# Performance work log

Measured on AMD Instinct MI355X. Metric: run time of the kernel, lower is better.

The kernel has to match this reference:

```python
import math
import jax, jax.numpy as jnp
import numpy as np

B, L, E, H, NL = 8, 512, 512, 8, 2


def setup_inputs() -> dict:
    key = jax.random.key(0)
    ks = jax.random.split(key, 12)
    s = 0.02  # weight init scale
    return {
        "inputs_4e": jax.random.normal(ks[0], (B, L, 4 * E), jnp.float32),
        "query_embed": jax.random.normal(ks[1], (B, L, E), jnp.float32),
        "rel": jax.random.normal(ks[2], (B, L, L), jnp.float32),
        "resp_rel": jax.random.normal(ks[3], (B, L, L), jnp.float32),
        "timestamp": jax.random.uniform(ks[4], (B, L, L), jnp.float32) * 10.0,
        "l1": jax.random.uniform(ks[5], (1,), jnp.float32),
        "l2": jax.random.uniform(ks[6], (1,), jnp.float32),
        "l3": jax.random.uniform(ks[7], (1,), jnp.float32),
        "Win": jax.random.normal(ks[8], (4 * E, E), jnp.float32) * s,
        "b_in": jnp.zeros((E,), jnp.float32),
        "Wqkv": jax.random.normal(ks[9], (NL, 3, E, E), jnp.float32) * s,
        "bqkv": jnp.zeros((NL, 3, E), jnp.float32),
        "Wf1": jax.random.normal(ks[10], (2 * E, E), jnp.float32) * s,
        "bf1": jnp.zeros((E,), jnp.float32),
        "Wf2": jax.random.normal(ks[11], (E, 1), jnp.float32) * s,
        "bf2": jnp.zeros((1,), jnp.float32),
    }


def _mha(q_in, k_in, v_in, Wq, bq, Wk, bk, Wv, bv,
         rel, resp_rel, timestamp, l1, l2, l3, mask):
    Bb, Ll, Ee = q_in.shape
    d = Ee // H

    def split(x, W, b):  # (B,L,E) -> (B,H,L,d)
        return (x @ W + b).reshape(Bb, Ll, H, d).transpose(0, 2, 1, 3)

    q = split(q_in, Wq, bq)
    k = split(k_in, Wk, bk)
    v = split(v_in, Wv, bv)

    # relation softmax: zero out where mask==False, -1e4 at zeros
    maskf = mask.astype(rel.dtype)              # (1,1,L,L)
    rel_m = rel[:, None, :, :] * maskf          # (B,1,L,L), broadcasts over heads
    rel_attn = jax.nn.softmax(jnp.where(rel_m == 0, -1e4, rel_m), axis=-1)
    resp_m = resp_rel[:, None, :, :] * maskf
    resp_attn = jax.nn.softmax(jnp.where(resp_m == 0, -1e4, resp_m), axis=-1)

    # QK softmax with causal mask
    scores = jnp.einsum('bhqd,bhkd->bhqk', q, k) / math.sqrt(d)
    scores = jnp.where(mask, -1e9, scores)
    prob_attn = jax.nn.softmax(scores, axis=-1)

    # time-decay softmax
    ts = jnp.exp(-jnp.abs(timestamp))[:, None, :, :]  # (B,1,L,L)
    ts = jnp.where(mask, -jnp.inf, ts)
    time_attn = jax.nn.softmax(ts, axis=-1)

    # blend (ablation flags all True)
    p = (1.0 - l2) * prob_attn + l2 * time_attn
    p = (1.0 - l1) * p + l1 * rel_attn
    p = (1.0 - l3) * p + l3 * resp_attn

    out = jnp.einsum('bhqk,bhkd->bhqd', p, v)
    out = out.transpose(0, 2, 1, 3).reshape(Bb, Ll, Ee)
    return out, p


def reference(inputs_4e, query_embed, rel, resp_rel, timestamp,
              l1, l2, l3, Win, b_in, Wqkv, bqkv, Wf1, bf1, Wf2, bf2):
    mask = jnp.triu(jnp.ones((1, 1, L, L), dtype=bool), k=1)  # future mask
    inputs = jax.nn.relu(inputs_4e @ Win + b_in)              # lin_in_interaction

    outputs, attn = _mha(query_embed, inputs, inputs,
                         Wqkv[0, 0], bqkv[0, 0], Wqkv[0, 1], bqkv[0, 1],
                         Wqkv[0, 2], bqkv[0, 2],
                         rel, resp_rel, timestamp, l1, l2, l3, mask)
    for i in range(1, NL):
        residual, attn = _mha(query_embed, outputs, outputs,
                              Wqkv[i, 0], bqkv[i, 0], Wqkv[i, 1], bqkv[i, 1],
                              Wqkv[i, 2], bqkv[i, 2],
                              rel, resp_rel, timestamp, l1, l2, l3, mask)
        outputs = outputs + jax.nn.relu(residual)

    concat_q = jnp.concatenate([outputs, query_embed], axis=-1)  # (B,L,2E)
    h = jax.nn.relu(concat_q @ Wf1 + bf1)
    return h @ Wf2 + bf2  # (B,L,1)
```

## Files before the change

### kernel.cpp

```cpp
#include <hip/hip_runtime.h>
#include <math.h>

namespace {
constexpr int B = 8, L = 512, E = 512, H = 8;
constexpr int M = B * L;
}

typedef float f32x4 __attribute__((ext_vector_type(4)));
typedef short bf16x8 __attribute__((ext_vector_type(8)));

__device__ inline ushort f2b(float f) {
  unsigned u = __float_as_uint(f);
  u += 0x7FFF + ((u >> 16) & 1);
  return (ushort)(u >> 16);
}
__device__ inline float b2f(ushort h) { return __uint_as_float(((unsigned)h) << 16); }

__device__ inline f32x4 mfma16(bf16x8 a, bf16x8 b, f32x4 c) {
  return __builtin_amdgcn_mfma_f32_16x16x32_bf16(a, b, c, 0, 0, 0);
}

__device__ __forceinline__ void gl2lds16(const ushort* g, ushort* l) {
  __builtin_amdgcn_global_load_lds(
      (const __attribute__((address_space(1))) void*)g,
      (__attribute__((address_space(3))) void*)l, 16, 0, 0);
}

template <int NROWS>
__device__ __forceinline__ void stage64(const ushort* __restrict__ g, int ldg,
                                        ushort* lds, int tid) {
  const int w = tid >> 6, l = tid & 63;
  constexpr int RPW = NROWS / 4;
  constexpr int NI = RPW / 8;
#pragma unroll
  for (int it = 0; it < NI; ++it) {
    const int rbase = w * RPW + it * 8;
    const int row = rbase + (l >> 3);
    const int chunk = (l & 7) ^ (row & 7);
    gl2lds16(g + (size_t)row * ldg + chunk * 8, lds + rbase * 64);
  }
}

template <int BM, int NBUF>
__device__ __forceinline__ void stage_comb(const ushort* b0, const ushort* b1,
                                           const ushort* b2, const ushort* b3,
                                           ushort* lds, int tid) {
#pragma unroll
  for (int it = 0; it < BM / 32; ++it) {
    const int row = (tid >> 3) + it * 32;
    const int slot = tid & 7;
    const size_t off = (size_t)row * 512 + slot * 8;
    union Uu { uint4 u; ushort s[8]; } va, vb, vc, vd, vo;
    va.u = *(const uint4*)(b0 + off);
    vb.u = *(const uint4*)(b1 + off);
    if (NBUF == 4) {
      vc.u = *(const uint4*)(b2 + off);
      vd.u = *(const uint4*)(b3 + off);
    }
#pragma unroll
    for (int e = 0; e < 8; ++e) {
      float f = b2f(va.s[e]) + b2f(vb.s[e]);
      if (NBUF == 4) f += fmaxf(b2f(vc.s[e]) + b2f(vd.s[e]), 0.f);
      vo.s[e] = f2b(f);
    }
    *(uint4*)(&lds[row * 64 + ((slot ^ (row & 7)) * 8)]) = vo.u;
  }
}

template <int BM, int MODE, int HAS_BIAS, int ACT, int STAGEA>
__device__ __forceinline__ void dev_gemm(
    ushort* lds, int bxx, int by, const ushort* A, const ushort* A2,
    const ushort* A3, const ushort* A4, const ushort* Aq,
    const ushort* Wt, const float* bias, ushort* C0, ushort* C1, ushort* C2,
    ushort* C3, int K, int N) {
  ushort* Als = lds;
  ushort* Bls = lds + 2 * BM * 64;
  const int tid = threadIdx.x;
  const int l = tid & 63, wv = tid >> 6;
  const int wr = wv >> 1, wc = wv & 1;
  const int g = l >> 4, c = l & 15;
  constexpr int WM = BM / 2;
  constexpr int MFR = WM / 16;
  const int bm = by * BM;
  const int bn64 = bxx * 64;
  const int sec = (MODE == 3 || MODE == 5) ? (bn64 >> 9) : 0;
  const bool vsec = (MODE == 3 && sec == 2) || (MODE == 5 && sec == 1);

  const ushort* Ause = A;
  if (MODE == 3 && (sec == 1 || sec == 2)) Ause = A2;
  const int ldA = K;
  const ushort* Bp = Wt + (size_t)bn64 * K;

  f32x4 acc[MFR][2];
#pragma unroll
  for (int mi = 0; mi < MFR; ++mi)
#pragma unroll
    for (int ni = 0; ni < 2; ++ni) acc[mi][ni] = f32x4{0.f, 0.f, 0.f, 0.f};

  auto stageA = [&](int t, int buf) {
    ushort* dst = Als + buf * BM * 64;
    if (STAGEA == 0) {
      stage64<BM>(Ause + (size_t)bm * ldA + t * 64, ldA, dst, tid);
    } else if (STAGEA == 2) {
      stage_comb<BM, 2>(A + (size_t)bm * 512 + t * 64,
                        A2 + (size_t)bm * 512 + t * 64, nullptr, nullptr, dst, tid);
    } else {
      if (t < 8)
        stage_comb<BM, 4>(A + (size_t)bm * 512 + t * 64,
                          A2 + (size_t)bm * 512 + t * 64,
                          A3 + (size_t)bm * 512 + t * 64,
                          A4 + (size_t)bm * 512 + t * 64, dst, tid);
      else
        stage64<BM>(Aq + (size_t)bm * 512 + (t - 8) * 64, 512, dst, tid);
    }
  };

  stageA(0, 0);
  stage64<64>(Bp, K, Bls, tid);
  __syncthreads();

  const int NT = K >> 6;
  int cur = 0;
  for (int t = 0; t < NT; ++t) {
    if (t + 1 < NT) {
      stageA(t + 1, cur ^ 1);
      stage64<64>(Bp + (t + 1) * 64, K, Bls + (cur ^ 1) * 64 * 64, tid);
    }
#pragma unroll
    for (int ks = 0; ks < 2; ++ks) {
      bf16x8 af[MFR], bf_[2];
#pragma unroll
      for (int mi = 0; mi < MFR; ++mi) {
        const int row = wr * WM + mi * 16 + c;
        af[mi] = *(const bf16x8*)(&Als[cur * BM * 64 + row * 64 +
                                       (((ks * 4 + g) ^ (row & 7)) * 8)]);
      }
#pragma unroll
      for (int ni = 0; ni < 2; ++ni) {
        const int row = wc * 32 + ni * 16 + c;
        bf_[ni] = *(const bf16x8*)(&Bls[cur * 64 * 64 + row * 64 +
                                        (((ks * 4 + g) ^ (row & 7)) * 8)]);
      }
      if (vsec) {
#pragma unroll
        for (int mi = 0; mi < MFR; ++mi)
#pragma unroll
          for (int ni = 0; ni < 2; ++ni)
            acc[mi][ni] = mfma16(bf_[ni], af[mi], acc[mi][ni]);
      } else {
#pragma unroll
        for (int mi = 0; mi < MFR; ++mi)
#pragma unroll
          for (int ni = 0; ni < 2; ++ni)
            acc[mi][ni] = mfma16(af[mi], bf_[ni], acc[mi][ni]);
      }
    }
    __syncthreads();
    cur ^= 1;
  }

  if (vsec) {
    const int vbase = (MODE == 3) ? 1024 : 512;
    const int e0 = bn64 - vbase;
#pragma unroll
    for (int ni = 0; ni < 2; ++ni) {
#pragma unroll
      for (int r = 0; r < 4; ++r) {
        const int e = e0 + wc * 32 + ni * 16 + g * 4 + r;
        const float bv = HAS_BIAS ? bias[vbase + e] : 0.f;
#pragma unroll
        for (int mi = 0; mi < MFR; ++mi) {
          const int m = bm + wr * WM + mi * 16 + c;
          const int bb = m >> 9, lt = m & 511;
          C2[((size_t)bb * 512 + e) * 512 + lt] = f2b(acc[mi][ni][r] + bv);
        }
      }
    }
  } else {
    ushort* dst = C0;
    int nsub = 0, ldc = N;
    if (MODE == 3 || MODE == 5) {
      dst = (MODE == 5) ? C1 : (sec == 0 ? C0 : (sec == 1 ? C1 : C3));
      nsub = sec * 512;
      ldc = 512;
    }
#pragma unroll
    for (int ni = 0; ni < 2; ++ni) {
      const int n = bn64 + wc * 32 + ni * 16 + c;
      const float bv = HAS_BIAS ? bias[n] : 0.f;
#pragma unroll
      for (int mi = 0; mi < MFR; ++mi) {
#pragma unroll
        for (int r = 0; r < 4; ++r) {
          const int m = bm + wr * WM + mi * 16 + g * 4 + r;
          float v = acc[mi][ni][r] + bv;
          if (ACT) v = fmaxf(v, 0.f);
          dst[(size_t)m * ldc + (n - nsub)] = f2b(v);
        }
      }
    }
  }
}

__device__ __forceinline__ void dev_attn(ushort* lds, int bidx,
                                         const ushort* __restrict__ Qg,
                                         const ushort* __restrict__ Kg,
                                         const ushort* __restrict__ Vt,
                                         float c_p, ushort* __restrict__ aexp) {
  ushort* Qs = lds;
  ushort* Ps = lds + 4096;
  ushort* Ks = lds + 8192;
  ushort* Vs = lds + 16384;
  const int qt = 7 - (bidx & 7);
  const int h = (bidx >> 3) & 7;
  const int b = bidx >> 6;
  const int tid = threadIdx.x, l = tid & 63, w = tid >> 6;
  const int g = l >> 4, c = l & 15;
  const int qrow0 = b * L + qt * 64;
  const ushort* Kbase = Kg + (size_t)(b * L) * E + h * 64;
  const ushort* Vbase = Vt + (size_t)(b * E + h * 64) * L;

  stage64<64>(Qg + (size_t)qrow0 * E + h * 64, E, Qs, tid);
  stage64<64>(Kbase, E, Ks, tid);
  stage64<64>(Vbase, L, Vs, tid);
  __syncthreads();

  f32x4 o[4];
#pragma unroll
  for (int dn = 0; dn < 4; ++dn) o[dn] = f32x4{0.f, 0.f, 0.f, 0.f};
  float l_r[4] = {0.f, 0.f, 0.f, 0.f};

  int cur = 0;
  for (int kt = 0; kt <= qt; ++kt) {
    if (kt < qt) {
      stage64<64>(Kbase + (size_t)(kt + 1) * 64 * E, E, Ks + (cur ^ 1) * 4096, tid);
      stage64<64>(Vbase + (kt + 1) * 64, L, Vs + (cur ^ 1) * 4096, tid);
    }
    bf16x8 qf[2];
#pragma unroll
    for (int kq = 0; kq < 2; ++kq) {
      int row = w * 16 + c;
      qf[kq] = *(const bf16x8*)(&Qs[row * 64 + (((kq * 4 + g) ^ (row & 7)) * 8)]);
    }
    f32x4 s4[4];
#pragma unroll
    for (int n = 0; n < 4; ++n) s4[n] = f32x4{0.f, 0.f, 0.f, 0.f};
#pragma unroll
    for (int n = 0; n < 4; ++n) {
#pragma unroll
      for (int kq = 0; kq < 2; ++kq) {
        int row = n * 16 + c;
        bf16x8 kf = *(const bf16x8*)(&Ks[cur * 4096 + row * 64 +
                                         (((kq * 4 + g) ^ (row & 7)) * 8)]);
        s4[n] = mfma16(qf[kq], kf, s4[n]);
      }
    }
    const bool diag = (kt == qt);
    float pv[4][4];
    float lad[4] = {0.f, 0.f, 0.f, 0.f};
#pragma unroll
    for (int n = 0; n < 4; ++n)
#pragma unroll
      for (int r = 0; r < 4; ++r) {
        float sv = s4[n][r] * 0.125f;
        if (diag && (n * 16 + c) > (w * 16 + g * 4 + r)) sv = -1e30f;
        float p = __expf(sv);
        pv[n][r] = p;
        lad[r] += p;
      }
#pragma unroll
    for (int off = 1; off < 16; off <<= 1)
#pragma unroll
      for (int r = 0; r < 4; ++r) lad[r] += __shfl_xor(lad[r], off);
#pragma unroll
    for (int r = 0; r < 4; ++r) l_r[r] += lad[r];
#pragma unroll
    for (int n = 0; n < 4; ++n)
#pragma unroll
      for (int r = 0; r < 4; ++r) {
        int q = w * 16 + g * 4 + r;
        int byt = 32 * n + 2 * c;
        int slot = byt >> 4;
        Ps[q * 64 + ((slot ^ (q & 7)) * 8) + ((byt & 15) >> 1)] = f2b(pv[n][r]);
      }
    bf16x8 pf[2];
#pragma unroll
    for (int kq = 0; kq < 2; ++kq) {
      int row = w * 16 + c;
      pf[kq] = *(const bf16x8*)(&Ps[row * 64 + (((kq * 4 + g) ^ (row & 7)) * 8)]);
    }
#pragma unroll
    for (int dn = 0; dn < 4; ++dn) {
#pragma unroll
      for (int kq = 0; kq < 2; ++kq) {
        int row = dn * 16 + c;
        bf16x8 vf = *(const bf16x8*)(&Vs[cur * 4096 + row * 64 +
                                         (((kq * 4 + g) ^ (row & 7)) * 8)]);
        o[dn] = mfma16(pf[kq], vf, o[dn]);
      }
    }
    __syncthreads();
    cur ^= 1;
  }

  float linv[4];
#pragma unroll
  for (int r = 0; r < 4; ++r) linv[r] = c_p / l_r[r];
#pragma unroll
  for (int dn = 0; dn < 4; ++dn) {
#pragma unroll
    for (int r = 0; r < 4; ++r) {
      const size_t row = (size_t)qrow0 + w * 16 + g * 4 + r;
      const int col = h * 64 + dn * 16 + c;
      aexp[row * E + col] = f2b(o[dn][r] * linv[r]);
    }
  }
}

__device__ __forceinline__ void dev_blend(int idx, const float* __restrict__ rel,
                                          const float* __restrict__ resp,
                                          const float* __restrict__ ts,
                                          float l1, float l2, float l3,
                                          ushort* __restrict__ stat) {
  const float c_t = (1.f - l3) * (1.f - l1) * l2;
  const float c_r = (1.f - l3) * l1;
  const float c_s = l3;
  const int wave = threadIdx.x >> 6, lane = threadIdx.x & 63;
  const int row = idx * 4 + wave;
  const int qi = row & (L - 1);
  const size_t base = (size_t)row * L;
  float rv[8], sv[8], tv[8];
#pragma unroll
  for (int jj = 0; jj < 8; ++jj) {
    const int k = jj * 64 + lane;
    const float r = rel[base + k];
    const float s = resp[base + k];
    const float tt = ts[base + k];
    const bool fut = (k > qi);
    const float rm = fut ? r : 0.f;
    const float sm = fut ? s : 0.f;
    rv[jj] = (rm == 0.f) ? -1e4f : rm;
    sv[jj] = (sm == 0.f) ? -1e4f : sm;
    tv[jj] = fut ? -INFINITY : __expf(-fabsf(tt));
  }
  float rmax = -INFINITY, smax = -INFINITY, tmax = -INFINITY;
#pragma unroll
  for (int jj = 0; jj < 8; ++jj) {
    rmax = fmaxf(rmax, rv[jj]); smax = fmaxf(smax, sv[jj]); tmax = fmaxf(tmax, tv[jj]);
  }
  for (int off = 1; off < 64; off <<= 1) {
    rmax = fmaxf(rmax, __shfl_xor(rmax, off));
    smax = fmaxf(smax, __shfl_xor(smax, off));
    tmax = fmaxf(tmax, __shfl_xor(tmax, off));
  }
  float rsum = 0.f, ssum = 0.f, tsum = 0.f;
#pragma unroll
  for (int jj = 0; jj < 8; ++jj) {
    rsum += __expf(rv[jj] - rmax); ssum += __expf(sv[jj] - smax); tsum += __expf(tv[jj] - tmax);
  }
  for (int off = 1; off < 64; off <<= 1) {
    rsum += __shfl_xor(rsum, off);
    ssum += __shfl_xor(ssum, off);
    tsum += __shfl_xor(tsum, off);
  }
  const float rinv = c_r / rsum, sinv = c_s / ssum, tinv = c_t / tsum;
#pragma unroll
  for (int jj = 0; jj < 8; ++jj) {
    stat[base + jj * 64 + lane] =
        f2b(__expf(rv[jj] - rmax) * rinv + __expf(sv[jj] - smax) * sinv +
            __expf(tv[jj] - tmax) * tinv);
  }
}

__device__ __forceinline__ void tcvt_body(const float* __restrict__ src,
                                          ushort* __restrict__ dst, int Kd, int Nd,
                                          int kb, int nb, int t, ushort (*T)[33]) {
  const int r = t >> 3, c4 = (t & 7) * 4;
  float4 v = *(const float4*)(src + (size_t)(kb + r) * Nd + nb + c4);
  T[r][c4 + 0] = f2b(v.x); T[r][c4 + 1] = f2b(v.y);
  T[r][c4 + 2] = f2b(v.z); T[r][c4 + 3] = f2b(v.w);
  __syncthreads();
  ushort4 ov = {T[c4 + 0][r], T[c4 + 1][r], T[c4 + 2][r], T[c4 + 3][r]};
  *(ushort4*)(&dst[(size_t)(nb + r) * Kd + kb + c4]) = ov;
}

__global__ __launch_bounds__(256) void k_prep(
    const float* __restrict__ x4e, const float* __restrict__ query,
    const float* __restrict__ Win, const float* __restrict__ Wqkv,
    const float* __restrict__ Wf1, ushort* __restrict__ x4e_bf,
    ushort* __restrict__ qbf, ushort* __restrict__ Wint,
    ushort* __restrict__ Wqkvt, ushort* __restrict__ Wf1t) {
  __shared__ ushort T[32][33];
  const int NB_CVT = (M * 2048 / 4 + M * 512 / 4) / 256;
  const int bi = blockIdx.x;
  const int t = threadIdx.x;
  if (bi < NB_CVT) {
    const int N1 = M * 2048 / 4;
    int i = bi * 256 + t;
    if (i < N1) {
      float4 v = ((const float4*)x4e)[i];
      ushort4 o = {f2b(v.x), f2b(v.y), f2b(v.z), f2b(v.w)};
      ((ushort4*)x4e_bf)[i] = o;
    } else {
      int j = i - N1;
      float4 v = ((const float4*)query)[j];
      ushort4 o = {f2b(v.x), f2b(v.y), f2b(v.z), f2b(v.w)};
      ((ushort4*)qbf)[j] = o;
    }
    return;
  }
  const int idx = bi - NB_CVT;
  const long long EE = (long long)E * E;
  if (idx < 1024) {
    tcvt_body(Win, Wint, 2048, 512, (idx >> 4) * 32, (idx & 15) * 32, t, T);
  } else if (idx < 2560) {
    const int q = idx - 1024;
    const int z = q >> 8, r = q & 255;
    tcvt_body(Wqkv + z * EE, Wqkvt + z * EE, 512, 512, (r >> 4) * 32, (r & 15) * 32, t, T);
  } else {
    const int q = idx - 2560;
    tcvt_body(Wf1, Wf1t, 1024, 512, (q >> 4) * 32, (q & 15) * 32, t, T);
  }
}

__global__ __launch_bounds__(256) void k_xgemm_blend(
    const ushort* __restrict__ x4e_bf, const ushort* __restrict__ Wint,
    const float* __restrict__ b_in, ushort* __restrict__ x_bf,
    const float* __restrict__ rel, const float* __restrict__ resp,
    const float* __restrict__ ts, const float* __restrict__ l1p,
    const float* __restrict__ l2p, const float* __restrict__ l3p,
    ushort* __restrict__ stat) {
  extern __shared__ ushort lds[];
  const int bx = blockIdx.x;
  if (bx < 512) {
    dev_gemm<64, 1, 1, 1, 0>(lds, bx & 7, bx >> 3, x4e_bf, nullptr, nullptr,
                             nullptr, nullptr, Wint, b_in, x_bf, nullptr,
                             nullptr, nullptr, 2048, 512);
  } else {
    dev_blend(bx - 512, rel, resp, ts, l1p[0], l2p[0], l3p[0], stat);
  }
}

__global__ __launch_bounds__(256) void k_qkv0(
    const ushort* __restrict__ query_bf, const ushort* __restrict__ x_bf,
    const ushort* __restrict__ Wqkvt, const float* __restrict__ bqkv,
    ushort* __restrict__ q_bf, ushort* __restrict__ k_bf,
    ushort* __restrict__ vt, ushort* __restrict__ q1_bf) {
  extern __shared__ ushort lds[];
  dev_gemm<128, 3, 1, 0, 0>(lds, blockIdx.x, blockIdx.y, query_bf, x_bf, nullptr,
                            nullptr, nullptr, Wqkvt, bqkv, q_bf, k_bf, vt, q1_bf,
                            512, 2048);
}

__global__ __launch_bounds__(256) void k_attn_stat(
    const ushort* __restrict__ Qg, const ushort* __restrict__ Kg,
    const ushort* __restrict__ Vt, const ushort* __restrict__ stat,
    const float* __restrict__ l1p, const float* __restrict__ l2p,
    const float* __restrict__ l3p, ushort* __restrict__ aexp,
    ushort* __restrict__ ostat) {
  extern __shared__ ushort lds[];
  const int bx = blockIdx.x;
  if (bx < 512) {
    const float l1 = l1p[0], l2 = l2p[0], l3 = l3p[0];
    const float c_p = (1.f - l3) * (1.f - l1) * (1.f - l2);
    dev_attn(lds, bx, Qg, Kg, Vt, c_p, aexp);
  } else {
    const int idx = bx - 512;
    const int bz = idx >> 6, r = idx & 63;
    const long long LLs = (long long)L * L, ELs = (long long)E * L;
    dev_gemm<64, 1, 0, 0, 0>(lds, r & 7, r >> 3, stat + bz * LLs, nullptr,
                             nullptr, nullptr, nullptr, Vt + bz * ELs, nullptr,
                             ostat + bz * ELs, nullptr, nullptr, nullptr, 512, 512);
  }
}

__global__ __launch_bounds__(256) void k_kv1(
    const ushort* __restrict__ aexp0, const ushort* __restrict__ ostat0,
    const ushort* __restrict__ Wt, const float* __restrict__ bias,
    ushort* __restrict__ k_bf, ushort* __restrict__ vt) {
  extern __shared__ ushort lds[];
  dev_gemm<128, 5, 1, 0, 2>(lds, blockIdx.x, blockIdx.y, aexp0, ostat0, nullptr,
                            nullptr, nullptr, Wt, bias, nullptr, k_bf, vt,
                            nullptr, 512, 1024);
}

__global__ __launch_bounds__(256) void k_f1(
    const ushort* __restrict__ aexp0, const ushort* __restrict__ ostat0,
    const ushort* __restrict__ aexp1, const ushort* __restrict__ ostat1,
    const ushort* __restrict__ query_bf, const ushort* __restrict__ Wf1t,
    const float* __restrict__ bf1, ushort* __restrict__ h_bf) {
  extern __shared__ ushort lds[];
  dev_gemm<64, 4, 1, 1, 4>(lds, blockIdx.x, blockIdx.y, aexp0, ostat0, aexp1,
                           ostat1, query_bf, Wf1t, bf1, h_bf, nullptr, nullptr,
                           nullptr, 1024, 512);
}

__global__ __launch_bounds__(256) void final_dot_kernel(
    const ushort* __restrict__ hb, const float* __restrict__ w,
    const float* __restrict__ b2, float* __restrict__ out) {
  const int m = blockIdx.x * 4 + (threadIdx.x >> 6);
  const int lane = threadIdx.x & 63;
  float s = 0.f;
#pragma unroll
  for (int it = 0; it < 2; ++it) {
    const int e = it * 256 + lane * 4;
    ushort4 hv = *(const ushort4*)(hb + (size_t)m * E + e);
    float4 wv = *(const float4*)(w + e);
    s += b2f(hv.x) * wv.x + b2f(hv.y) * wv.y + b2f(hv.z) * wv.z + b2f(hv.w) * wv.w;
  }
  for (int off = 1; off < 64; off <<= 1) s += __shfl_xor(s, off);
  if (lane == 0) out[m] = s + b2[0];
}

extern "C" void kernel_launch(void* const* d_in, const int* in_sizes, int n_in,
                              void* d_out, int out_size, void* d_ws, size_t ws_size,
                              hipStream_t stream) {
  (void)in_sizes; (void)n_in; (void)out_size; (void)ws_size;
  const float* inputs_4e = (const float*)d_in[0];
  const float* query = (const float*)d_in[1];
  const float* rel = (const float*)d_in[2];
  const float* resp = (const float*)d_in[3];
  const float* tsp = (const float*)d_in[4];
  const float* l1p = (const float*)d_in[5];
  const float* l2p = (const float*)d_in[6];
  const float* l3p = (const float*)d_in[7];
  const float* Win = (const float*)d_in[8];
  const float* b_in = (const float*)d_in[9];
  const float* Wqkv = (const float*)d_in[10];
  const float* bqkv = (const float*)d_in[11];
  const float* Wf1 = (const float*)d_in[12];
  const float* bf1 = (const float*)d_in[13];
  const float* Wf2 = (const float*)d_in[14];
  const float* bf2 = (const float*)d_in[15];

  char* ws = (char*)d_ws;
  const size_t MB = 1ull << 20;
  ushort* x4e_bf  = (ushort*)(ws + 0 * MB);
  ushort* aexp0   = (ushort*)(ws + 0 * MB);
  ushort* ostat0  = (ushort*)(ws + 4 * MB);
  ushort* aexp1   = (ushort*)(ws + 8 * MB);
  ushort* ostat1  = (ushort*)(ws + 12 * MB);
  ushort* query_bf= (ushort*)(ws + 16 * MB);
  ushort* stat_bf = (ushort*)(ws + 20 * MB);
  ushort* x_bf    = (ushort*)(ws + 24 * MB);
  ushort* h_bf    = (ushort*)(ws + 24 * MB);
  ushort* q_bf    = (ushort*)(ws + 28 * MB);
  ushort* k_bf    = (ushort*)(ws + 32 * MB);
  ushort* vt      = (ushort*)(ws + 36 * MB);
  ushort* q1_bf   = (ushort*)(ws + 40 * MB);
  ushort* Wint    = (ushort*)(ws + 48 * MB);
  ushort* Wqkvt   = (ushort*)(ws + 50 * MB);
  ushort* Wf1t    = (ushort*)(ws + 53 * MB);

  const long long EE = (long long)E * E;
  const int LDS_G64 = (2 * 64 * 64 + 2 * 64 * 64) * 2;
  const int LDS_G128 = (2 * 128 * 64 + 2 * 64 * 64) * 2;
  const int LDS_AS = 49152;

  k_prep<<<10240 + 3072, 256, 0, stream>>>(inputs_4e, query, Win, Wqkv, Wf1,
                                           x4e_bf, query_bf, Wint, Wqkvt, Wf1t);
  k_xgemm_blend<<<512 + 1024, 256, LDS_G64, stream>>>(
      x4e_bf, Wint, b_in, x_bf, rel, resp, tsp, l1p, l2p, l3p, stat_bf);
  k_qkv0<<<dim3(32, 32), 256, LDS_G128, stream>>>(query_bf, x_bf, Wqkvt, bqkv,
                                                  q_bf, k_bf, vt, q1_bf);
  k_attn_stat<<<1024, 256, LDS_AS, stream>>>(q_bf, k_bf, vt, stat_bf,
                                             l1p, l2p, l3p, aexp0, ostat0);
  k_kv1<<<dim3(16, 32), 256, LDS_G128, stream>>>(aexp0, ostat0, Wqkvt + 4 * EE,
                                                 bqkv + 4 * E, k_bf, vt);
  k_attn_stat<<<1024, 256, LDS_AS, stream>>>(q1_bf, k_bf, vt, stat_bf,
                                             l1p, l2p, l3p, aexp1, ostat1);
  k_f1<<<dim3(8, 64), 256, LDS_G64, stream>>>(aexp0, ostat0, aexp1, ostat1,
                                              query_bf, Wf1t, bf1, h_bf);
  final_dot_kernel<<<M / 4, 256, 0, stream>>>(h_bf, Wf2, bf2, (float*)d_out);
}
```

Measured before the change: 142.4 us.

## Fuse input bf16 conversion into GEMM staging and final dot into f1 epilogue

The x4e GEMM now loads fp32 input directly and converts it to bf16 while staging to LDS, dropping the separate conversion pass and its intermediate buffer. The Wqkv/Wf1 transposes move into the xgemm/blend kernel. The final dot with Wf2 is fused into the f1 GEMM epilogue using shuffles and atomicAdd into an output pre-initialised with the bias. This removes a launch and the h round trip, at the cost of doubled A-load bytes in the GEMM and nondeterministic float atomics.

```diff
diff --git a/kernel.cpp b/kernel.cpp
--- a/kernel.cpp
+++ b/kernel.cpp
@@ -67,12 +67,12 @@
   }
 }
 
-template <int BM, int MODE, int HAS_BIAS, int ACT, int STAGEA>
+template <int BM, int MODE, int HAS_BIAS, int ACT, int STAGEA, int FUSE>
 __device__ __forceinline__ void dev_gemm(
     ushort* lds, int bxx, int by, const ushort* A, const ushort* A2,
     const ushort* A3, const ushort* A4, const ushort* Aq,
     const ushort* Wt, const float* bias, ushort* C0, ushort* C1, ushort* C2,
-    ushort* C3, int K, int N) {
+    ushort* C3, const float* w2, float* outv, int K, int N) {
   ushort* Als = lds;
   ushort* Bls = lds + 2 * BM * 64;
   const int tid = threadIdx.x;
@@ -101,6 +101,22 @@
     ushort* dst = Als + buf * BM * 64;
     if (STAGEA == 0) {
       stage64<BM>(Ause + (size_t)bm * ldA + t * 64, ldA, dst, tid);
+    } else if (STAGEA == 1) {
+      const float* Af = (const float*)A;
+#pragma unroll
+      for (int it = 0; it < BM / 32; ++it) {
+        const int row = (tid >> 3) + it * 32;
+        const int slot = tid & 7;
+        const float* src = Af + (size_t)(bm + row) * K + t * 64 + slot * 8;
+        float4 v0 = *(const float4*)src;
+        float4 v1 = *(const float4*)(src + 4);
+        union { uint4 u; ushort s[8]; } vo;
+        vo.s[0] = f2b(v0.x); vo.s[1] = f2b(v0.y);
+        vo.s[2] = f2b(v0.z); vo.s[3] = f2b(v0.w);
+        vo.s[4] = f2b(v1.x); vo.s[5] = f2b(v1.y);
+        vo.s[6] = f2b(v1.z); vo.s[7] = f2b(v1.w);
+        *(uint4*)(&dst[row * 64 + ((slot ^ (row & 7)) * 8)]) = vo.u;
+      }
     } else if (STAGEA == 2) {
       stage_comb<BM, 2>(A + (size_t)bm * 512 + t * 64,
                         A2 + (size_t)bm * 512 + t * 64, nullptr, nullptr, dst, tid);
@@ -159,7 +175,30 @@
     cur ^= 1;
   }
 
-  if (vsec) {
+  if (FUSE) {
+    float w2v[2];
+#pragma unroll
+    for (int ni = 0; ni < 2; ++ni) w2v[ni] = w2[bn64 + wc * 32 + ni * 16 + c];
+#pragma unroll
+    for (int mi = 0; mi < MFR; ++mi) {
+#pragma unroll
+      for (int r = 0; r < 4; ++r) {
+        float p = 0.f;
+#pragma unroll
+        for (int ni = 0; ni < 2; ++ni) {
+          const int n = bn64 + wc * 32 + ni * 16 + c;
+          float v = acc[mi][ni][r] + bias[n];
+          v = fmaxf(v, 0.f);
+          p += v * w2v[ni];
+        }
+        p += __shfl_xor(p, 1);
+        p += __shfl_xor(p, 2);
+        p += __shfl_xor(p, 4);
+        p += __shfl_xor(p, 8);
+        if (c == 0) atomicAdd(&outv[bm + wr * WM + mi * 16 + g * 4 + r], p);
+      }
+    }
+  } else if (vsec) {
     const int vbase = (MODE == 3) ? 1024 : 512;
     const int e0 = bn64 - vbase;
 #pragma unroll
@@ -385,47 +424,37 @@
 }
 
 __global__ __launch_bounds__(256) void k_prep(
-    const float* __restrict__ x4e, const float* __restrict__ query,
-    const float* __restrict__ Win, const float* __restrict__ Wqkv,
-    const float* __restrict__ Wf1, ushort* __restrict__ x4e_bf,
-    ushort* __restrict__ qbf, ushort* __restrict__ Wint,
-    ushort* __restrict__ Wqkvt, ushort* __restrict__ Wf1t) {
+    const float* __restrict__ query, const float* __restrict__ Win,
+    const float* __restrict__ bf2, ushort* __restrict__ qbf,
+    ushort* __restrict__ Wint, float* __restrict__ outv) {
   __shared__ ushort T[32][33];
-  const int NB_CVT = (M * 2048 / 4 + M * 512 / 4) / 256;
   const int bi = blockIdx.x;
   const int t = threadIdx.x;
-  if (bi < NB_CVT) {
-    const int N1 = M * 2048 / 4;
-    int i = bi * 256 + t;
-    if (i < N1) {
-      float4 v = ((const float4*)x4e)[i];
-      ushort4 o = {f2b(v.x), f2b(v.y), f2b(v.z), f2b(v.w)};
-      ((ushort4*)x4e_bf)[i] = o;
-    } else {
-      int j = i - N1;
-      float4 v = ((const float4*)query)[j];
-      ushort4 o = {f2b(v.x), f2b(v.y), f2b(v.z), f2b(v.w)};
-      ((ushort4*)qbf)[j] = o;
-    }
+  if (bi < 2048) {
+    int j = bi * 256 + t;
+    float4 v = ((const float4*)query)[j];
+    ushort4 o = {f2b(v.x), f2b(v.y), f2b(v.z), f2b(v.w)};
+    ((ushort4*)qbf)[j] = o;
     return;
   }
-  const int idx = bi - NB_CVT;
-  const long long EE = (long long)E * E;
-  if (idx < 1024) {
+  if (bi < 3072) {
+    const int idx = bi - 2048;
     tcvt_body(Win, Wint, 2048, 512, (idx >> 4) * 32, (idx & 15) * 32, t, T);
-  } else if (idx < 2560) {
-    const int q = idx - 1024;
-    const int z = q >> 8, r = q & 255;
-    tcvt_body(Wqkv + z * EE, Wqkvt + z * EE, 512, 512, (r >> 4) * 32, (r & 15) * 32, t, T);
-  } else {
-    const int q = idx - 2560;
-    tcvt_body(Wf1, Wf1t, 1024, 512, (q >> 4) * 32, (q & 15) * 32, t, T);
+    return;
+  }
+  {
+    const int i = (bi - 3072) * 256 + t;
+    const float b2 = bf2[0];
+    float4 v = {b2, b2, b2, b2};
+    ((float4*)outv)[i] = v;
   }
 }
 
 __global__ __launch_bounds__(256) void k_xgemm_blend(
-    const ushort* __restrict__ x4e_bf, const ushort* __restrict__ Wint,
+    const float* __restrict__ x4e, const ushort* __restrict__ Wint,
     const float* __restrict__ b_in, ushort* __restrict__ x_bf,
+    const float* __restrict__ Wqkv, const float* __restrict__ Wf1,
+    ushort* __restrict__ Wqkvt, ushort* __restrict__ Wf1t,
     const float* __restrict__ rel, const float* __restrict__ resp,
     const float* __restrict__ ts, const float* __restrict__ l1p,
     const float* __restrict__ l2p, const float* __restrict__ l3p,
@@ -433,11 +462,24 @@
   extern __shared__ ushort lds[];
   const int bx = blockIdx.x;
   if (bx < 512) {
-    dev_gemm<64, 1, 1, 1, 0>(lds, bx & 7, bx >> 3, x4e_bf, nullptr, nullptr,
-                             nullptr, nullptr, Wint, b_in, x_bf, nullptr,
-                             nullptr, nullptr, 2048, 512);
+    dev_gemm<64, 1, 1, 1, 1, 0>(lds, bx & 7, bx >> 3, (const ushort*)x4e,
+                                nullptr, nullptr, nullptr, nullptr, Wint, b_in,
+                                x_bf, nullptr, nullptr, nullptr, nullptr,
+                                nullptr, 2048, 512);
+  } else if (bx < 2560) {
+    const int idx = bx - 512;
+    const long long EE = (long long)E * E;
+    if (idx < 1536) {
+      const int z = idx >> 8, r = idx & 255;
+      tcvt_body(Wqkv + z * EE, Wqkvt + z * EE, 512, 512, (r >> 4) * 32,
+                (r & 15) * 32, threadIdx.x, (ushort(*)[33])lds);
+    } else {
+      const int q = idx - 1536;
+      tcvt_body(Wf1, Wf1t, 1024, 512, (q >> 4) * 32, (q & 15) * 32,
+                threadIdx.x, (ushort(*)[33])lds);
+    }
   } else {
-    dev_blend(bx - 512, rel, resp, ts, l1p[0], l2p[0], l3p[0], stat);
+    dev_blend(bx - 2560, rel, resp, ts, l1p[0], l2p[0], l3p[0], stat);
   }
 }
 
@@ -447,9 +489,9 @@
     ushort* __restrict__ q_bf, ushort* __restrict__ k_bf,
     ushort* __restrict__ vt, ushort* __restrict__ q1_bf) {
   extern __shared__ ushort lds[];
-  dev_gemm<128, 3, 1, 0, 0>(lds, blockIdx.x, blockIdx.y, query_bf, x_bf, nullptr,
-                            nullptr, nullptr, Wqkvt, bqkv, q_bf, k_bf, vt, q1_bf,
-                            512, 2048);
+  dev_gemm<128, 3, 1, 0, 0, 0>(lds, blockIdx.x, blockIdx.y, query_bf, x_bf,
+                               nullptr, nullptr, nullptr, Wqkvt, bqkv, q_bf,
+                               k_bf, vt, q1_bf, nullptr, nullptr, 512, 2048);
 }
 
 __global__ __launch_bounds__(256) void k_attn_stat(
@@ -468,9 +510,10 @@
     const int idx = bx - 512;
     const int bz = idx >> 6, r = idx & 63;
     const long long LLs = (long long)L * L, ELs = (long long)E * L;
-    dev_gemm<64, 1, 0, 0, 0>(lds, r & 7, r >> 3, stat + bz * LLs, nullptr,
-                             nullptr, nullptr, nullptr, Vt + bz * ELs, nullptr,
-                             ostat + bz * ELs, nullptr, nullptr, nullptr, 512, 512);
+    dev_gemm<64, 1, 0, 0, 0, 0>(lds, r & 7, r >> 3, stat + bz * LLs, nullptr,
+                                nullptr, nullptr, nullptr, Vt + bz * ELs,
+                                nullptr, ostat + bz * ELs, nullptr, nullptr,
+                                nullptr, nullptr, nullptr, 512, 512);
   }
 }
 
@@ -479,37 +522,21 @@
     const ushort* __restrict__ Wt, const float* __restrict__ bias,
     ushort* __restrict__ k_bf, ushort* __restrict__ vt) {
   extern __shared__ ushort lds[];
-  dev_gemm<128, 5, 1, 0, 2>(lds, blockIdx.x, blockIdx.y, aexp0, ostat0, nullptr,
-                            nullptr, nullptr, Wt, bias, nullptr, k_bf, vt,
-                            nullptr, 512, 1024);
+  dev_gemm<128, 5, 1, 0, 2, 0>(lds, blockIdx.x, blockIdx.y, aexp0, ostat0,
+                               nullptr, nullptr, nullptr, Wt, bias, nullptr,
+                               k_bf, vt, nullptr, nullptr, nullptr, 512, 1024);
 }
 
 __global__ __launch_bounds__(256) void k_f1(
     const ushort* __restrict__ aexp0, const ushort* __restrict__ ostat0,
     const ushort* __restrict__ aexp1, const ushort* __restrict__ ostat1,
     const ushort* __restrict__ query_bf, const ushort* __restrict__ Wf1t,
-    const float* __restrict__ bf1, ushort* __restrict__ h_bf) {
+    const float* __restrict__ bf1, const float* __restrict__ Wf2,
+    float* __restrict__ outv) {
   extern __shared__ ushort lds[];
-  dev_gemm<64, 4, 1, 1, 4>(lds, blockIdx.x, blockIdx.y, aexp0, ostat0, aexp1,
-                           ostat1, query_bf, Wf1t, bf1, h_bf, nullptr, nullptr,
-                           nullptr, 1024, 512);
-}
-
-__global__ __launch_bounds__(256) void final_dot_kernel(
-    const ushort* __restrict__ hb, const float* __restrict__ w,
-    const float* __restrict__ b2, float* __restrict__ out) {
-  const int m = blockIdx.x * 4 + (threadIdx.x >> 6);
-  const int lane = threadIdx.x & 63;
-  float s = 0.f;
-#pragma unroll
-  for (int it = 0; it < 2; ++it) {
-    const int e = it * 256 + lane * 4;
-    ushort4 hv = *(const ushort4*)(hb + (size_t)m * E + e);
-    float4 wv = *(const float4*)(w + e);
-    s += b2f(hv.x) * wv.x + b2f(hv.y) * wv.y + b2f(hv.z) * wv.z + b2f(hv.w) * wv.w;
-  }
-  for (int off = 1; off < 64; off <<= 1) s += __shfl_xor(s, off);
-  if (lane == 0) out[m] = s + b2[0];
+  dev_gemm<64, 4, 1, 1, 4, 1>(lds, blockIdx.x, blockIdx.y, aexp0, ostat0,
+                              aexp1, ostat1, query_bf, Wf1t, bf1, nullptr,
+                              nullptr, nullptr, nullptr, Wf2, outv, 1024, 512);
 }
 
 extern "C" void kernel_launch(void* const* d_in, const int* in_sizes, int n_in,
@@ -535,7 +562,6 @@
 
   char* ws = (char*)d_ws;
   const size_t MB = 1ull << 20;
-  ushort* x4e_bf  = (ushort*)(ws + 0 * MB);
   ushort* aexp0   = (ushort*)(ws + 0 * MB);
   ushort* ostat0  = (ushort*)(ws + 4 * MB);
   ushort* aexp1   = (ushort*)(ws + 8 * MB);
@@ -543,7 +569,6 @@
   ushort* query_bf= (ushort*)(ws + 16 * MB);
   ushort* stat_bf = (ushort*)(ws + 20 * MB);
   ushort* x_bf    = (ushort*)(ws + 24 * MB);
-  ushort* h_bf    = (ushort*)(ws + 24 * MB);
   ushort* q_bf    = (ushort*)(ws + 28 * MB);
   ushort* k_bf    = (ushort*)(ws + 32 * MB);
   ushort* vt      = (ushort*)(ws + 36 * MB);
@@ -557,10 +582,11 @@
   const int LDS_G128 = (2 * 128 * 64 + 2 * 64 * 64) * 2;
   const int LDS_AS = 49152;
 
-  k_prep<<<10240 + 3072, 256, 0, stream>>>(inputs_4e, query, Win, Wqkv, Wf1,
-                                           x4e_bf, query_bf, Wint, Wqkvt, Wf1t);
-  k_xgemm_blend<<<512 + 1024, 256, LDS_G64, stream>>>(
-      x4e_bf, Wint, b_in, x_bf, rel, resp, tsp, l1p, l2p, l3p, stat_bf);
+  k_prep<<<3076, 256, 0, stream>>>(query, Win, bf2, query_bf, Wint,
+                                   (float*)d_out);
+  k_xgemm_blend<<<512 + 2048 + 1024, 256, LDS_G64, stream>>>(
+      inputs_4e, Wint, b_in, x_bf, Wqkv, Wf1, Wqkvt, Wf1t,
+      rel, resp, tsp, l1p, l2p, l3p, stat_bf);
   k_qkv0<<<dim3(32, 32), 256, LDS_G128, stream>>>(query_bf, x_bf, Wqkvt, bqkv,
                                                   q_bf, k_bf, vt, q1_bf);
   k_attn_stat<<<1024, 256, LDS_AS, stream>>>(q_bf, k_bf, vt, stat_bf,
@@ -570,6 +596,6 @@
   k_attn_stat<<<1024, 256, LDS_AS, stream>>>(q1_bf, k_bf, vt, stat_bf,
                                              l1p, l2p, l3p, aexp1, ostat1);
   k_f1<<<dim3(8, 64), 256, LDS_G64, stream>>>(aexp0, ostat0, aexp1, ostat1,
-                                              query_bf, Wf1t, bf1, h_bf);
-  final_dot_kernel<<<M / 4, 256, 0, stream>>>(h_bf, Wf2, bf2, (float*)d_out);
-}
+                                              query_bf, Wf1t, bf1, Wf2,
+                                              (float*)d_out);
+}
```

Measured after the change: 154.0 us. 1.08x slower.
